# Performance work log

Hardware: AMD Instinct MI355X
Metric: run time of the kernel (lower is better)

The kernel has to match this reference:

```python
import jax, jax.numpy as jnp
import numpy as np

N = 30000
NUM_FEAT = 129   # data.x.shape[1] + 1
NUM_CLASSES = 40
HID = 64

def _gat_conv(x, src, dst, W, a_src, a_dst, bias):
    """PyG GATConv (concat=True, negative_slope=0.2), self-loops pre-added to src/dst."""
    n = x.shape[0]
    H, C = a_src.shape
    h = (x @ W).reshape(n, H, C)                       # [N,H,C]
    alpha_s = jnp.sum(h * a_src[None], axis=-1)        # [N,H]
    alpha_d = jnp.sum(h * a_dst[None], axis=-1)        # [N,H]
    e = jax.nn.leaky_relu(alpha_s[src] + alpha_d[dst], 0.2)   # [E,H]
    m = jax.ops.segment_max(e, dst, num_segments=n)
    m = jnp.where(jnp.isfinite(m), m, 0.0)
    ex = jnp.exp(e - m[dst])
    denom = jax.ops.segment_sum(ex, dst, num_segments=n)
    alpha = ex / (denom[dst] + 1e-16)                  # segment softmax over in-edges
    out = jax.ops.segment_sum(h[src] * alpha[:, :, None], dst, num_segments=n)
    return out.reshape(n, H * C) + bias


def setup_inputs() -> dict:
    key = jax.random.key(0)
    ks = jax.random.split(key, 16)
    E = 480000
    x = jax.random.normal(ks[0], (N, NUM_FEAT), dtype=jnp.float32)
    edge_index = jax.random.randint(ks[1], (2, E), 0, N, dtype=jnp.int64)
    def w(k, shape, fan_in):
        return (jax.random.normal(k, shape, dtype=jnp.float32) * (1.0 / np.sqrt(fan_in))).astype(jnp.float32)
    # conv1: in=129, H=7, C=64
    W1 = w(ks[2], (NUM_FEAT, 7 * HID), NUM_FEAT)
    a1s = w(ks[3], (7, HID), HID); a1d = w(ks[4], (7, HID), HID)
    b1 = jnp.zeros((7 * HID,), jnp.float32)
    # conv2: in=448, H=6, C=64
    W2 = w(ks[5], (7 * HID, 6 * HID), 7 * HID)
    a2s = w(ks[6], (6, HID), HID); a2d = w(ks[7], (6, HID), HID)
    b2 = jnp.zeros((6 * HID,), jnp.float32)
    # conv3: in=384, H=6, C=40
    W3 = w(ks[8], (6 * HID, 6 * NUM_CLASSES), 6 * HID)
    a3s = w(ks[9], (6, NUM_CLASSES), NUM_CLASSES); a3d = w(ks[10], (6, NUM_CLASSES), NUM_CLASSES)
    b3 = jnp.zeros((6 * NUM_CLASSES,), jnp.float32)
    return {"x": x, "edge_index": edge_index,
            "W1": W1, "a1s": a1s, "a1d": a1d, "b1": b1,
            "W2": W2, "a2s": a2s, "a2d": a2d, "b2": b2,
            "W3": W3, "a3s": a3s, "a3d": a3d, "b3": b3}


def reference(x, edge_index, W1, a1s, a1d, b1, W2, a2s, a2d, b2, W3, a3s, a3d, b3):
    n = x.shape[0]
    loop = jnp.arange(n, dtype=edge_index.dtype)
    src = jnp.concatenate([edge_index[0], loop])   # PyG add_self_loops=True
    dst = jnp.concatenate([edge_index[1], loop])
    # dropout is identity in eval mode
    h = _gat_conv(x, src, dst, W1, a1s, a1d, b1)
    h = jax.nn.relu(h)
    h = _gat_conv(h, src, dst, W2, a2s, a2d, b2)
    h = jax.nn.relu(h)
    out = _gat_conv(h, src, dst, W3, a3s, a3d, b3)
    return out
```

## Files before the change

### kernel.cpp

```cpp
#include <hip/hip_runtime.h>
#include <hip/hip_bf16.h>


#define NFEAT 129
#define MPAD  30080

typedef __attribute__((ext_vector_type(8))) short short8v;
typedef __attribute__((ext_vector_type(8))) unsigned short u16x8;
typedef __attribute__((ext_vector_type(8))) __bf16 bf16x8;
typedef __attribute__((ext_vector_type(4))) float f32x4;
typedef unsigned short u16;

union FragU { short8v s; bf16x8 b; };

__device__ inline u16 f2bf(float x) {
    unsigned u = __builtin_bit_cast(unsigned, x);
    unsigned r = (u + 0x7fffu + ((u >> 16) & 1u)) >> 16;
    return (u16)r;
}
__device__ inline float bf2f(u16 b) {
    unsigned u = ((unsigned)b) << 16;
    return __builtin_bit_cast(float, u);
}
__device__ inline float h2f(u16 u) { return (float)__builtin_bit_cast(_Float16, u); }
__device__ inline u16 f2h(float v) { return __builtin_bit_cast(u16, (_Float16)v); }


__global__ __launch_bounds__(256) void init_cnt_k(int* __restrict__ cnt, int n) {
    int i = blockIdx.x * 256 + threadIdx.x;
    if (i < n) cnt[i] = 1;
}

__global__ __launch_bounds__(256) void hist_k(const int* __restrict__ dst, int* __restrict__ cnt, int E) {
    int e = blockIdx.x * 256 + threadIdx.x;
    if (e < E) atomicAdd(&cnt[dst[e]], 1);
}

__global__ __launch_bounds__(1024) void scan_k(const int* __restrict__ cnt, int* __restrict__ row_ptr, int n) {
    __shared__ int part[1024];
    int tid = threadIdx.x;
    int per = (n + 1023) >> 10;
    int base = tid * per;
    int s = 0;
    for (int j = 0; j < per; ++j) {
        int idx = base + j;
        if (idx < n) s += cnt[idx];
    }
    part[tid] = s;
    __syncthreads();
    for (int off = 1; off < 1024; off <<= 1) {
        int v = 0;
        if (tid >= off) v = part[tid - off];
        __syncthreads();
        if (tid >= off) part[tid] += v;
        __syncthreads();
    }
    int run = (tid > 0) ? part[tid - 1] : 0;
    for (int j = 0; j < per; ++j) {
        int idx = base + j;
        if (idx < n) { row_ptr[idx] = run; run += cnt[idx]; }
    }
    if (tid == 0) row_ptr[n] = part[1023];
}

__global__ __launch_bounds__(256) void scatter_k(const int* __restrict__ src, const int* __restrict__ dst,
                                                 const int* __restrict__ row_ptr, int* __restrict__ fill,
                                                 int* __restrict__ col, int E, int n) {
    int e = blockIdx.x * 256 + threadIdx.x;
    if (e < E + n) {
        int s, d;
        if (e < E) { s = src[e]; d = dst[e]; }
        else       { s = d = e - E; }
        int pos = row_ptr[d] + atomicAdd(&fill[d], 1);
        col[pos] = s;
    }
}


__global__ __launch_bounds__(256) void xsplit_k(const float* __restrict__ in,
                                                u16* __restrict__ hi, u16* __restrict__ lo,
                                                int Nn, int K, int Kp, int Mp) {
    int idx = blockIdx.x * 256 + threadIdx.x;
    if (idx >= Mp * Kp) return;
    int m = idx / Kp, k = idx - m * Kp;
    float v = (m < Nn && k < K) ? in[(size_t)m * K + k] : 0.f;
    u16 h = f2bf(v);
    hi[idx] = h;
    lo[idx] = f2bf(v - bf2f(h));
}


__global__ __launch_bounds__(256) void wsplitAll_k(const float* __restrict__ W1,
                                                   const float* __restrict__ W2,
                                                   const float* __restrict__ W3,
                                                   u16* __restrict__ hi, u16* __restrict__ lo) {
    int idx = blockIdx.x * 256 + threadIdx.x;
    if (idx >= 352256) return;
    const float* W; int loc, Kp, K, N;
    if (idx < 81920)       { W = W1; loc = idx;          Kp = 160; K = 129; N = 448; }
    else if (idx < 253952) { W = W2; loc = idx - 81920;  Kp = 448; K = 448; N = 384; }
    else                   { W = W3; loc = idx - 253952; Kp = 384; K = 384; N = 240; }
    int nn = loc / Kp, k = loc - nn * Kp;
    float v = (k < K && nn < N) ? W[(size_t)k * N + nn] : 0.f;
    u16 h = f2bf(v);
    hi[idx] = h;
    lo[idx] = f2bf(v - bf2f(h));
}


__global__ __launch_bounds__(256) void projAll_k(
    const float* __restrict__ W1, const float* __restrict__ a1s, const float* __restrict__ a1d,
    const float* __restrict__ W2, const float* __restrict__ a2s, const float* __restrict__ a2d,
    const float* __restrict__ W3, const float* __restrict__ a3s, const float* __restrict__ a3d,
    float* __restrict__ Ps, float* __restrict__ Pd) {
    int idx = blockIdx.x * 256 + threadIdx.x;
    if (idx >= 992 * 8) return;
    int row = idx >> 3, h = idx & 7;
    const float *W, *as_, *ad_; int k, K, Ncols, H, C;
    if (row < 160)      { k = row;       K = 129; W = W1; as_ = a1s; ad_ = a1d; Ncols = 448; H = 7; C = 64; }
    else if (row < 608) { k = row - 160; K = 448; W = W2; as_ = a2s; ad_ = a2d; Ncols = 384; H = 6; C = 64; }
    else                { k = row - 608; K = 384; W = W3; as_ = a3s; ad_ = a3d; Ncols = 240; H = 6; C = 40; }
    float ps = 0.f, pd = 0.f;
    if (h < H && k < K) {
        const float* wr = W + (size_t)k * Ncols + h * C;
        const float* ar = as_ + h * C;
        const float* dr = ad_ + h * C;
        for (int c = 0; c < C; ++c) {
            float wv = wr[c];
            ps += wv * ar[c];
            pd += wv * dr[c];
        }
    }
    Ps[idx] = ps;
    Pd[idx] = pd;
}


__global__ __launch_bounds__(256) void zeropads_k(u16* __restrict__ h1hi, u16* __restrict__ h1lo,
                                                  int Nn) {
    int tot = (MPAD - Nn) * 448;
    int idx = blockIdx.x * 256 + threadIdx.x;
    if (idx < tot) {
        h1hi[(size_t)Nn * 448 + idx] = 0;
        h1lo[(size_t)Nn * 448 + idx] = 0;
    }
}


__global__ __launch_bounds__(256) void alpha1_k(const float* __restrict__ x,
                                                const float* __restrict__ Ps,
                                                const float* __restrict__ Pd,
                                                float* __restrict__ oS, float* __restrict__ oD, int n) {
    int wv = threadIdx.x >> 6, lane = threadIdx.x & 63;
    int i = blockIdx.x * 4 + wv;
    if (i >= n) return;
    const float* row = x + (size_t)i * NFEAT;
    float x0 = row[lane], x1 = row[64 + lane];
    float ps[8], pd[8];
    #pragma unroll
    for (int h = 0; h < 8; ++h) {
        ps[h] = x0 * Ps[lane * 8 + h] + x1 * Ps[(64 + lane) * 8 + h];
        pd[h] = x0 * Pd[lane * 8 + h] + x1 * Pd[(64 + lane) * 8 + h];
    }
    if (lane == 0) {
        float x2 = row[128];
        #pragma unroll
        for (int h = 0; h < 8; ++h) {
            ps[h] += x2 * Ps[128 * 8 + h];
            pd[h] += x2 * Pd[128 * 8 + h];
        }
    }
    #pragma unroll
    for (int h = 0; h < 8; ++h) {
        #pragma unroll
        for (int off = 32; off; off >>= 1) {
            ps[h] += __shfl_xor(ps[h], off);
            pd[h] += __shfl_xor(pd[h], off);
        }
    }
    if (lane == 0) {
        #pragma unroll
        for (int h = 0; h < 8; ++h) {
            oS[(size_t)i * 8 + h] = ps[h];
            oD[(size_t)i * 8 + h] = pd[h];
        }
    }
}


__device__ __forceinline__ int swz(int r, int s) {
    return (r << 2) | ((s ^ (r & 3) ^ ((r >> 2) & 3)) & 3);
}


__global__ __launch_bounds__(256) void gemm16(
    const u16* __restrict__ Ahi, const u16* __restrict__ Alo,
    const u16* __restrict__ Bhi, const u16* __restrict__ Blo,
    u16* __restrict__ C16, int M, int Ncols, int Kp)
{
    __shared__ __align__(16) u16 sAh[128 * 32];
    __shared__ __align__(16) u16 sAl[128 * 32];
    __shared__ __align__(16) u16 sBh[128 * 32];
    __shared__ __align__(16) u16 sBl[128 * 32];
    const int tid = threadIdx.x;
    const int m0 = blockIdx.y * 128;
    const int n0 = blockIdx.x * 128;
    const int lane = tid & 63, wave = tid >> 6;
    const int wm = wave >> 1, wn = wave & 1;
    const int l15 = lane & 15, lg = lane >> 4;
    const int r0 = tid >> 2, s0 = tid & 3;
    const int w0 = swz(r0, s0), w1 = swz(r0 + 64, s0);
    f32x4 acc[4][4] = {};

    for (int k0 = 0; k0 < Kp; k0 += 32) {
        size_t gA0 = (size_t)(m0 + r0) * Kp + k0 + s0 * 8;
        size_t gA1 = (size_t)(m0 + r0 + 64) * Kp + k0 + s0 * 8;
        size_t gB0 = (size_t)(n0 + r0) * Kp + k0 + s0 * 8;
        size_t gB1 = (size_t)(n0 + r0 + 64) * Kp + k0 + s0 * 8;
        short8v ah0 = *(const short8v*)(Ahi + gA0);
        short8v ah1 = *(const short8v*)(Ahi + gA1);
        short8v al0 = *(const short8v*)(Alo + gA0);
        short8v al1 = *(const short8v*)(Alo + gA1);
        short8v bh0 = *(const short8v*)(Bhi + gB0);
        short8v bh1 = *(const short8v*)(Bhi + gB1);
        short8v bl0 = *(const short8v*)(Blo + gB0);
        short8v bl1 = *(const short8v*)(Blo + gB1);
        __syncthreads();
        ((short8v*)sAh)[w0] = ah0; ((short8v*)sAh)[w1] = ah1;
        ((short8v*)sAl)[w0] = al0; ((short8v*)sAl)[w1] = al1;
        ((short8v*)sBh)[w0] = bh0; ((short8v*)sBh)[w1] = bh1;
        ((short8v*)sBl)[w0] = bl0; ((short8v*)sBl)[w1] = bl1;
        __syncthreads();
        FragU fah[4], fal[4], fbh[4], fbl[4];
        #pragma unroll
        for (int mf = 0; mf < 4; ++mf) {
            int rr = wm * 64 + mf * 16 + l15;
            int idx = swz(rr, lg);
            fah[mf].s = ((const short8v*)sAh)[idx];
            fal[mf].s = ((const short8v*)sAl)[idx];
        }
        #pragma unroll
        for (int nf = 0; nf < 4; ++nf) {
            int rr = wn * 64 + nf * 16 + l15;
            int idx = swz(rr, lg);
            fbh[nf].s = ((const short8v*)sBh)[idx];
            fbl[nf].s = ((const short8v*)sBl)[idx];
        }
        #pragma unroll
        for (int mf = 0; mf < 4; ++mf) {
            #pragma unroll
            for (int nf = 0; nf < 4; ++nf) {
                acc[mf][nf] = __builtin_amdgcn_mfma_f32_16x16x32_bf16(fah[mf].b, fbh[nf].b, acc[mf][nf], 0, 0, 0);
                acc[mf][nf] = __builtin_amdgcn_mfma_f32_16x16x32_bf16(fah[mf].b, fbl[nf].b, acc[mf][nf], 0, 0, 0);
                acc[mf][nf] = __builtin_amdgcn_mfma_f32_16x16x32_bf16(fal[mf].b, fbh[nf].b, acc[mf][nf], 0, 0, 0);
            }
        }
    }
    #pragma unroll
    for (int mf = 0; mf < 4; ++mf) {
        #pragma unroll
        for (int nf = 0; nf < 4; ++nf) {
            int colg = n0 + wn * 64 + nf * 16 + l15;
            if (colg >= Ncols) continue;
            #pragma unroll
            for (int r = 0; r < 4; ++r) {
                int rowg = m0 + wm * 64 + mf * 16 + lg * 4 + r;
                if (rowg < M) C16[(size_t)rowg * Ncols + colg] = f2h(acc[mf][nf][r]);
            }
        }
    }
}


template <int H, int C, bool RELU, bool SPLIT, bool PROJ>
__global__ __launch_bounds__(256) void aggF_k(
    const u16* __restrict__ hf,
    const float* __restrict__ as_, const float* __restrict__ ad_,
    const float* __restrict__ bias,
    const int* __restrict__ row_ptr, const int* __restrict__ col,
    const float* __restrict__ Pns, const float* __restrict__ Pnd,
    float* __restrict__ nas, float* __restrict__ nad,
    float* __restrict__ outf, u16* __restrict__ ohi, u16* __restrict__ olo,
    int n)
{
    constexpr int HC = H * C;
    constexpr int LACT = HC / 8;
    const int wv = threadIdx.x >> 6, lane = threadIdx.x & 63;
    const int i = blockIdx.x * 4 + wv;
    if (i >= n) return;
    const int ch0 = lane * 8;
    const bool act = lane < LACT;
    const int h = act ? (ch0 / C) : 0;
    const bool lead = act && ((ch0 % C) == 0);
    const int beg = row_ptr[i], end = row_ptr[i + 1];
    float acc[8] = {};
    float dp = 0.f;
    if (act) {
        const float adh = ad_[(size_t)i * 8 + h];
        int e = beg;
        for (; e + 2 <= end; e += 2) {
            int sA = col[e], sB = col[e + 1];
            float fA = as_[(size_t)sA * 8 + h] + adh;
            float fB = as_[(size_t)sB * 8 + h] + adh;
            u16x8 vA = *(const u16x8*)(hf + (size_t)sA * HC + ch0);
            u16x8 vB = *(const u16x8*)(hf + (size_t)sB * HC + ch0);
            fA = fA > 0.f ? fA : 0.2f * fA;
            fB = fB > 0.f ? fB : 0.2f * fB;
            float wA = __expf(fA), wB = __expf(fB);
            #pragma unroll
            for (int j = 0; j < 8; ++j)
                acc[j] += wA * h2f(vA[j]) + wB * h2f(vB[j]);
            if (lead) dp += wA + wB;
        }
        if (e < end) {
            int sA = col[e];
            float fA = as_[(size_t)sA * 8 + h] + adh;
            u16x8 vA = *(const u16x8*)(hf + (size_t)sA * HC + ch0);
            fA = fA > 0.f ? fA : 0.2f * fA;
            float wA = __expf(fA);
            #pragma unroll
            for (int j = 0; j < 8; ++j)
                acc[j] += wA * h2f(vA[j]);
            if (lead) dp += wA;
        }
    }
    const float den = __shfl(dp, h * (C / 8)) + 1e-16f;
    float o[8];
    #pragma unroll
    for (int j = 0; j < 8; ++j) o[j] = 0.f;
    if (act) {
        #pragma unroll
        for (int j = 0; j < 8; ++j) {
            float v = acc[j] / den + bias[ch0 + j];
            if (RELU) v = fmaxf(v, 0.f);
            o[j] = v;
        }
        size_t base = (size_t)i * HC + ch0;
        if constexpr (SPLIT) {
            u16x8 ph, pl;
            #pragma unroll
            for (int j = 0; j < 8; ++j) {
                u16 hi = f2bf(o[j]);
                ph[j] = hi;
                pl[j] = f2bf(o[j] - bf2f(hi));
            }
            *(u16x8*)(ohi + base) = ph;
            *(u16x8*)(olo + base) = pl;
        } else {
            float4 q0; q0.x = o[0]; q0.y = o[1]; q0.z = o[2]; q0.w = o[3];
            float4 q1; q1.x = o[4]; q1.y = o[5]; q1.z = o[6]; q1.w = o[7];
            *(float4*)(outf + base) = q0;
            *(float4*)(outf + base + 4) = q1;
        }
    }
    if constexpr (PROJ) {
        float ps[8] = {}, pd[8] = {};
        if (act) {
            #pragma unroll
            for (int j = 0; j < 8; ++j) {
                const float* prs = Pns + (size_t)(ch0 + j) * 8;
                const float* prd = Pnd + (size_t)(ch0 + j) * 8;
                #pragma unroll
                for (int hp = 0; hp < 8; ++hp) {
                    ps[hp] += o[j] * prs[hp];
                    pd[hp] += o[j] * prd[hp];
                }
            }
        }
        #pragma unroll
        for (int hp = 0; hp < 8; ++hp) {
            #pragma unroll
            for (int off = 32; off; off >>= 1) {
                ps[hp] += __shfl_xor(ps[hp], off);
                pd[hp] += __shfl_xor(pd[hp], off);
            }
        }
        if (lane == 0) {
            #pragma unroll
            for (int hp = 0; hp < 8; ++hp) {
                nas[(size_t)i * 8 + hp] = ps[hp];
                nad[(size_t)i * 8 + hp] = pd[hp];
            }
        }
    }
}


extern "C" void kernel_launch(void* const* d_in, const int* in_sizes, int n_in,
                              void* d_out, int out_size, void* d_ws, size_t ws_size,
                              hipStream_t stream) {
    const float* x   = (const float*)d_in[0];
    const int*   ei  = (const int*)d_in[1];
    const float* W1  = (const float*)d_in[2];
    const float* a1s = (const float*)d_in[3];
    const float* a1d = (const float*)d_in[4];
    const float* b1  = (const float*)d_in[5];
    const float* W2  = (const float*)d_in[6];
    const float* a2s = (const float*)d_in[7];
    const float* a2d = (const float*)d_in[8];
    const float* b2  = (const float*)d_in[9];
    const float* W3  = (const float*)d_in[10];
    const float* a3s = (const float*)d_in[11];
    const float* a3d = (const float*)d_in[12];
    const float* b3  = (const float*)d_in[13];
    float* out = (float*)d_out;

    const int Nn = in_sizes[0] / NFEAT;
    const int E  = in_sizes[1] / 2;
    const int Et = E + Nn;
    const int* srcp = ei;
    const int* dstp = ei + E;

    char* ws = (char*)d_ws;
    size_t off = 0;
    auto carve = [&](size_t bytes) -> char* {
        char* p = ws + off;
        off += (bytes + 255) & ~(size_t)255;
        return p;
    };
    u16*   hbuf16 = (u16*)carve((size_t)MPAD * 448 * 2);
    u16*   h1hi  = (u16*)carve((size_t)MPAD * 448 * 2);
    u16*   h1lo  = (u16*)carve((size_t)MPAD * 448 * 2);
    u16*   Xhi   = (u16*)carve((size_t)MPAD * 160 * 2);
    u16*   Xlo   = (u16*)carve((size_t)MPAD * 160 * 2);
    u16*   Wthi  = (u16*)carve((size_t)352256 * 2);
    u16*   Wtlo  = (u16*)carve((size_t)352256 * 2);
    int*   col   = (int*)carve((size_t)Et * 4);
    int* row_ptr = (int*)carve((size_t)(Nn + 1) * 4);
    int*   cnt   = (int*)carve((size_t)Nn * 4);
    float* aA    = (float*)carve((size_t)Nn * 8 * 4);
    float* dA    = (float*)carve((size_t)Nn * 8 * 4);
    float* aB    = (float*)carve((size_t)Nn * 8 * 4);
    float* dB    = (float*)carve((size_t)Nn * 8 * 4);
    float* Ps    = (float*)carve((size_t)992 * 8 * 4);
    float* Pd    = (float*)carve((size_t)992 * 8 * 4);
    (void)ws_size;

    const int nb4 = (Nn + 3) / 4;
    const int mg  = MPAD / 128;

    init_cnt_k<<<(Nn + 255) / 256, 256, 0, stream>>>(cnt, Nn);
    hist_k<<<(E + 255) / 256, 256, 0, stream>>>(dstp, cnt, E);
    scan_k<<<1, 1024, 0, stream>>>(cnt, row_ptr, Nn);
    hipMemsetAsync(cnt, 0, (size_t)Nn * 4, stream);
    scatter_k<<<(Et + 255) / 256, 256, 0, stream>>>(srcp, dstp, row_ptr, cnt, col, E, Nn);

    xsplit_k<<<((MPAD * 160) + 255) / 256, 256, 0, stream>>>(x, Xhi, Xlo, Nn, NFEAT, 160, MPAD);
    wsplitAll_k<<<(352256 + 255) / 256, 256, 0, stream>>>(W1, W2, W3, Wthi, Wtlo);
    projAll_k<<<(992 * 8 + 255) / 256, 256, 0, stream>>>(W1, a1s, a1d, W2, a2s, a2d, W3, a3s, a3d, Ps, Pd);
    zeropads_k<<<(((MPAD - Nn) * 448) + 255) / 256, 256, 0, stream>>>(h1hi, h1lo, Nn);

    alpha1_k<<<nb4, 256, 0, stream>>>(x, Ps, Pd, aA, dA, Nn);
    gemm16<<<dim3(4, mg), 256, 0, stream>>>(Xhi, Xlo, Wthi, Wtlo, hbuf16, Nn, 448, 160);
    aggF_k<7, 64, true, true, true><<<nb4, 256, 0, stream>>>(
        hbuf16, aA, dA, b1, row_ptr, col, Ps + 1280, Pd + 1280, aB, dB,
        nullptr, h1hi, h1lo, Nn);

    gemm16<<<dim3(3, mg), 256, 0, stream>>>(h1hi, h1lo, Wthi + 81920, Wtlo + 81920, hbuf16, Nn, 384, 448);
    aggF_k<6, 64, true, true, true><<<nb4, 256, 0, stream>>>(
        hbuf16, aB, dB, b2, row_ptr, col, Ps + 4864, Pd + 4864, aA, dA,
        nullptr, h1hi, h1lo, Nn);

    gemm16<<<dim3(2, mg), 256, 0, stream>>>(h1hi, h1lo, Wthi + 253952, Wtlo + 253952, hbuf16, Nn, 240, 384);
    aggF_k<6, 40, false, false, false><<<nb4, 256, 0, stream>>>(
        hbuf16, aA, dA, b3, row_ptr, col, nullptr, nullptr, nullptr, nullptr,
        out, nullptr, nullptr, Nn);
}
```

Before: 602.8 us.

## Precompute normalized edge weights and split each node's aggregation across two waves

Adds a wnorm kernel that computes softmax-normalized attention weights per edge and head into a workspace buffer, using 8 edge slots × 8 heads per wave. The aggregation kernel then reads these weights instead of recomputing exp and the denominator. It assigns two waves per node, each taking alternate edges with a 4-way unrolled loop, and combines the partial sums through shared memory. This raises memory-level parallelism on the gather, at the cost of an extra kernel per layer and roughly 15 MB of weight traffic written and read back.

```diff
diff --git a/kernel.cpp b/kernel.cpp
--- a/kernel.cpp
+++ b/kernel.cpp
@@ -188,6 +188,37 @@
 }
 
 
+__global__ __launch_bounds__(256) void wnorm_k(const float* __restrict__ as_,
+                                               const float* __restrict__ ad_,
+                                               const int* __restrict__ row_ptr,
+                                               const int* __restrict__ col,
+                                               float* __restrict__ wn, int n) {
+    int wv = threadIdx.x >> 6, lane = threadIdx.x & 63;
+    int i = blockIdx.x * 4 + wv;
+    if (i >= n) return;
+    const int h = lane & 7, slot = lane >> 3;
+    const int beg = row_ptr[i], end = row_ptr[i + 1];
+    const float adh = ad_[(size_t)i * 8 + h];
+    float dp = 0.f;
+    for (int e = beg + slot; e < end; e += 8) {
+        int s = col[e];
+        float v = as_[(size_t)s * 8 + h] + adh;
+        v = v > 0.f ? v : 0.2f * v;
+        dp += __expf(v);
+    }
+    dp += __shfl_xor(dp, 8);
+    dp += __shfl_xor(dp, 16);
+    dp += __shfl_xor(dp, 32);
+    const float rinv = 1.f / (dp + 1e-16f);
+    for (int e = beg + slot; e < end; e += 8) {
+        int s = col[e];
+        float v = as_[(size_t)s * 8 + h] + adh;
+        v = v > 0.f ? v : 0.2f * v;
+        wn[(size_t)e * 8 + h] = __expf(v) * rinv;
+    }
+}
+
+
 __device__ __forceinline__ int swz(int r, int s) {
     return (r << 2) | ((s ^ (r & 3) ^ ((r >> 2) & 3)) & 3);
 }
@@ -273,9 +304,9 @@
 
 
 template <int H, int C, bool RELU, bool SPLIT, bool PROJ>
-__global__ __launch_bounds__(256) void aggF_k(
+__global__ __launch_bounds__(256) void aggG_k(
     const u16* __restrict__ hf,
-    const float* __restrict__ as_, const float* __restrict__ ad_,
+    const float* __restrict__ wn,
     const float* __restrict__ bias,
     const int* __restrict__ row_ptr, const int* __restrict__ col,
     const float* __restrict__ Pns, const float* __restrict__ Pnd,
@@ -285,57 +316,60 @@
 {
     constexpr int HC = H * C;
     constexpr int LACT = HC / 8;
+    __shared__ float lacc[2][LACT][8];
     const int wv = threadIdx.x >> 6, lane = threadIdx.x & 63;
-    const int i = blockIdx.x * 4 + wv;
-    if (i >= n) return;
+    const int node = blockIdx.x * 2 + (wv >> 1);
+    const int half = wv & 1;
     const int ch0 = lane * 8;
-    const bool act = lane < LACT;
-    const int h = act ? (ch0 / C) : 0;
-    const bool lead = act && ((ch0 % C) == 0);
-    const int beg = row_ptr[i], end = row_ptr[i + 1];
+    const bool act = (node < n) && (lane < LACT);
+    const int h = (lane < LACT) ? (ch0 / C) : 0;
     float acc[8] = {};
-    float dp = 0.f;
     if (act) {
-        const float adh = ad_[(size_t)i * 8 + h];
-        int e = beg;
-        for (; e + 2 <= end; e += 2) {
-            int sA = col[e], sB = col[e + 1];
-            float fA = as_[(size_t)sA * 8 + h] + adh;
-            float fB = as_[(size_t)sB * 8 + h] + adh;
+        const int beg = row_ptr[node], end = row_ptr[node + 1];
+        int e = beg + half;
+        for (; e + 6 < end; e += 8) {
+            int sA = col[e],     sB = col[e + 2];
+            int sC = col[e + 4], sD = col[e + 6];
+            float wA = wn[(size_t)e * 8 + h];
+            float wB = wn[(size_t)(e + 2) * 8 + h];
+            float wC = wn[(size_t)(e + 4) * 8 + h];
+            float wD = wn[(size_t)(e + 6) * 8 + h];
             u16x8 vA = *(const u16x8*)(hf + (size_t)sA * HC + ch0);
             u16x8 vB = *(const u16x8*)(hf + (size_t)sB * HC + ch0);
-            fA = fA > 0.f ? fA : 0.2f * fA;
-            fB = fB > 0.f ? fB : 0.2f * fB;
-            float wA = __expf(fA), wB = __expf(fB);
+            u16x8 vC = *(const u16x8*)(hf + (size_t)sC * HC + ch0);
+            u16x8 vD = *(const u16x8*)(hf + (size_t)sD * HC + ch0);
             #pragma unroll
             for (int j = 0; j < 8; ++j)
-                acc[j] += wA * h2f(vA[j]) + wB * h2f(vB[j]);
-            if (lead) dp += wA + wB;
-        }
-        if (e < end) {
+                acc[j] += wA * h2f(vA[j]) + wB * h2f(vB[j])
+                        + wC * h2f(vC[j]) + wD * h2f(vD[j]);
+        }
+        for (; e < end; e += 2) {
             int sA = col[e];
-            float fA = as_[(size_t)sA * 8 + h] + adh;
+            float wA = wn[(size_t)e * 8 + h];
             u16x8 vA = *(const u16x8*)(hf + (size_t)sA * HC + ch0);
-            fA = fA > 0.f ? fA : 0.2f * fA;
-            float wA = __expf(fA);
             #pragma unroll
             for (int j = 0; j < 8; ++j)
                 acc[j] += wA * h2f(vA[j]);
-            if (lead) dp += wA;
-        }
-    }
-    const float den = __shfl(dp, h * (C / 8)) + 1e-16f;
+        }
+    }
+    if (half == 1 && act) {
+        #pragma unroll
+        for (int j = 0; j < 8; ++j) lacc[wv >> 1][lane][j] = acc[j];
+    }
+    __syncthreads();
+    if (half == 1) return;
+
     float o[8];
     #pragma unroll
     for (int j = 0; j < 8; ++j) o[j] = 0.f;
     if (act) {
         #pragma unroll
         for (int j = 0; j < 8; ++j) {
-            float v = acc[j] / den + bias[ch0 + j];
+            float v = acc[j] + lacc[wv >> 1][lane][j] + bias[ch0 + j];
             if (RELU) v = fmaxf(v, 0.f);
             o[j] = v;
         }
-        size_t base = (size_t)i * HC + ch0;
+        size_t base = (size_t)node * HC + ch0;
         if constexpr (SPLIT) {
             u16x8 ph, pl;
             #pragma unroll
@@ -375,11 +409,11 @@
                 pd[hp] += __shfl_xor(pd[hp], off);
             }
         }
-        if (lane == 0) {
+        if (lane == 0 && node < n) {
             #pragma unroll
             for (int hp = 0; hp < 8; ++hp) {
-                nas[(size_t)i * 8 + hp] = ps[hp];
-                nad[(size_t)i * 8 + hp] = pd[hp];
+                nas[(size_t)node * 8 + hp] = ps[hp];
+                nad[(size_t)node * 8 + hp] = pd[hp];
             }
         }
     }
@@ -425,6 +459,7 @@
     u16*   Xlo   = (u16*)carve((size_t)MPAD * 160 * 2);
     u16*   Wthi  = (u16*)carve((size_t)352256 * 2);
     u16*   Wtlo  = (u16*)carve((size_t)352256 * 2);
+    float* wbuf  = (float*)carve((size_t)Et * 8 * 4);
     int*   col   = (int*)carve((size_t)Et * 4);
     int* row_ptr = (int*)carve((size_t)(Nn + 1) * 4);
     int*   cnt   = (int*)carve((size_t)Nn * 4);
@@ -437,6 +472,7 @@
     (void)ws_size;
 
     const int nb4 = (Nn + 3) / 4;
+    const int nb2 = (Nn + 1) / 2;
     const int mg  = MPAD / 128;
 
     init_cnt_k<<<(Nn + 255) / 256, 256, 0, stream>>>(cnt, Nn);
@@ -451,18 +487,21 @@
     zeropads_k<<<(((MPAD - Nn) * 448) + 255) / 256, 256, 0, stream>>>(h1hi, h1lo, Nn);
 
     alpha1_k<<<nb4, 256, 0, stream>>>(x, Ps, Pd, aA, dA, Nn);
+    wnorm_k<<<nb4, 256, 0, stream>>>(aA, dA, row_ptr, col, wbuf, Nn);
     gemm16<<<dim3(4, mg), 256, 0, stream>>>(Xhi, Xlo, Wthi, Wtlo, hbuf16, Nn, 448, 160);
-    aggF_k<7, 64, true, true, true><<<nb4, 256, 0, stream>>>(
-        hbuf16, aA, dA, b1, row_ptr, col, Ps + 1280, Pd + 1280, aB, dB,
+    aggG_k<7, 64, true, true, true><<<nb2, 256, 0, stream>>>(
+        hbuf16, wbuf, b1, row_ptr, col, Ps + 1280, Pd + 1280, aB, dB,
         nullptr, h1hi, h1lo, Nn);
 
+    wnorm_k<<<nb4, 256, 0, stream>>>(aB, dB, row_ptr, col, wbuf, Nn);
     gemm16<<<dim3(3, mg), 256, 0, stream>>>(h1hi, h1lo, Wthi + 81920, Wtlo + 81920, hbuf16, Nn, 384, 448);
-    aggF_k<6, 64, true, true, true><<<nb4, 256, 0, stream>>>(
-        hbuf16, aB, dB, b2, row_ptr, col, Ps + 4864, Pd + 4864, aA, dA,
+    aggG_k<6, 64, true, true, true><<<nb2, 256, 0, stream>>>(
+        hbuf16, wbuf, b2, row_ptr, col, Ps + 4864, Pd + 4864, aA, dA,
         nullptr, h1hi, h1lo, Nn);
 
+    wnorm_k<<<nb4, 256, 0, stream>>>(aA, dA, row_ptr, col, wbuf, Nn);
     gemm16<<<dim3(2, mg), 256, 0, stream>>>(h1hi, h1lo, Wthi + 253952, Wtlo + 253952, hbuf16, Nn, 240, 384);
-    aggF_k<6, 40, false, false, false><<<nb4, 256, 0, stream>>>(
-        hbuf16, aA, dA, b3, row_ptr, col, nullptr, nullptr, nullptr, nullptr,
+    aggG_k<6, 40, false, false, false><<<nb2, 256, 0, stream>>>(
+        hbuf16, wbuf, b3, row_ptr, col, nullptr, nullptr, nullptr, nullptr,
         out, nullptr, nullptr, Nn);
 }
```

New measurement: 641.9 us. 6.5% more time.
